# Kernel tuning notes

Hardware: AMD Instinct MI355X
Metric: run time of the kernel (lower is better)

The kernel has to match this reference:

```python
import jax, jax.numpy as jnp
import numpy as np

# model dims
N = 512        # node_size (ROIs)
S = 64         # sampling_size
TRS = 20       # TRs_per_window
STEPS = 20     # steps_per_TR = tr / step_size
DT = 0.05      # step_size (s)

# fixed Wong-Wang / Balloon-Windkessel constants (var=0 params in ParamsModel)
W_E, W_I = 1.0, 0.7
TAU_E, TAU_I = 0.1, 0.01
GAMMA_E, GAMMA_I = 0.641, 1.0
I_0, I_EXT = 0.32, 0.02
A_E, B_E, D_E = 310.0, 125.0, 0.16
A_I, B_I, D_I = 615.0, 177.0, 0.087
ALPHA, RHO = 0.32, 0.34
K1, K2, K3 = 2.38, 2.0, 0.48
V0, E0 = 0.02, 0.34
TAU_S, TAU_F, TAU_0 = 0.65, 0.41, 0.98


def h_tf(a, b, d, z):
    # abs-regularized sigmoid transfer (a*z-b)/(1-exp(-d*(a*z-b)))
    x = a * z - b
    return (1e-5 + jnp.abs(x)) / (1e-5 * d + jnp.abs(1.0 - jnp.exp(-d * x)))


def setup_inputs() -> dict:
    key = jax.random.key(0)
    ks = jax.random.split(key, 8)
    sc = jax.random.uniform(ks[0], (N, N), dtype=jnp.float32) * (1.0 - jnp.eye(N, dtype=jnp.float32))
    gains_con = 0.05 * jax.random.normal(ks[1], (N, N), dtype=jnp.float32)
    # hx: [N, 6] initial states (E, I, x, f, v, q)
    hx = jnp.concatenate([
        0.1 * jnp.ones((N, 2), jnp.float32),   # E, I
        jnp.zeros((N, 1), jnp.float32),        # x
        jnp.ones((N, 3), jnp.float32),         # f, v, q
    ], axis=1)
    hE = 0.1 * jnp.ones((N, 20), jnp.float32)
    external = jnp.zeros((N, STEPS, TRS), jnp.float32)
    noise_E0 = jax.random.normal(ks[2], (TRS, STEPS, N, S), dtype=jnp.float32)
    noise_I0 = jax.random.normal(ks[3], (TRS, STEPS, N, S), dtype=jnp.float32)
    noise_E = jax.random.normal(ks[4], (TRS, STEPS, N, S), dtype=jnp.float32)
    noise_I = jax.random.normal(ks[5], (TRS, STEPS, N, S), dtype=jnp.float32)
    noise_bold = jax.random.normal(ks[6], (TRS, N), dtype=jnp.float32)
    return dict(external=external, hx=hx, hE=hE, sc=sc, gains_con=gains_con,
                g=jnp.float32(20.0), g_EE=jnp.float32(3.5), g_IE=jnp.float32(0.42),
                g_EI=jnp.float32(0.42), std_in=jnp.float32(0.0), std_out=jnp.float32(0.02),
                noise_E0=noise_E0, noise_I0=noise_I0, noise_E=noise_E, noise_I=noise_I,
                noise_bold=noise_bold)


def reference(external, hx, hE, sc, gains_con, g, g_EE, g_IE, g_EI, std_in, std_out,
              noise_E0, noise_I0, noise_E, noise_I, noise_bold):
    relu = jax.nn.relu
    g_EE_e = 0.001 + relu(g_EE)
    g_IE_e = 0.001 + relu(g_IE)
    g_EI_e = 0.001 + relu(g_EI)
    std_in_e = 0.02 + relu(std_in)
    std_out_e = relu(std_out)
    # fitted, symmetrized, normalized SC -> Laplacian coupling
    sc_mod = jnp.exp(gains_con) * sc
    w = 0.5 * (sc_mod + sc_mod.T)
    w_n = w / jnp.linalg.norm(w)
    lap = -jnp.diag(w_n.sum(1)) + w_n                      # [N, N]
    ext = jnp.transpose(external, (2, 1, 0))               # [TRS, STEPS, N]
    sqdt = jnp.sqrt(jnp.float32(DT))

    def micro(carry, xs):
        hxE, hxI, x, f, v, q = carry
        e0, i0, eE, eI, ex = xs
        E = hxE[:, None] + 0.02 * e0                       # [N, S]
        I = hxI[:, None] + 0.001 * i0
        IE = jnp.tanh(relu(W_E * I_0 + I_EXT * ex[:, None] + g_EE_e * E + g * (lap @ E) - g_IE_e * I))
        II = jnp.tanh(relu(W_I * I_0 + g_EI_e * E - I))
        rE = h_tf(A_E, B_E, D_E, IE)
        rI = h_tf(A_I, B_I, D_I, II)
        En = E + DT * (-E / TAU_E + GAMMA_E * (1.0 - E) * rE) + sqdt * std_in_e * eE
        In = I + DT * (-I / TAU_I + GAMMA_I * rI) + sqdt * std_in_e * eI
        E = jnp.tanh(relu(En))                             # dynamic boundary
        I = jnp.tanh(relu(In))
        Em = jnp.maximum(E.mean(1), 1e-5)                  # [N]
        Im = jnp.maximum(I.mean(1), 1e-5)
        # hemodynamic (balloon-windkessel) states
        v_a = v ** (1.0 / ALPHA)
        xn = x + DT * (Em - x / TAU_S - (f - 1.0) / TAU_F)
        fn = f + DT * x
        vn = v + DT * (f - v_a) / TAU_0
        qn = q + DT * (f * (1.0 - (1.0 - RHO) ** (1.0 / f)) / RHO - q * v_a / v) / TAU_0
        return (Em, Im, jnp.tanh(xn), 1.0 + jnp.tanh(fn - 1.0),
                1.0 + jnp.tanh(vn - 1.0), 1.0 + jnp.tanh(qn - 1.0)), None

    def tr_step(carry, xs):
        e0, i0, eE, eI, exs, eb = xs
        carry, _ = jax.lax.scan(micro, carry, (e0, i0, eE, eI, exs))
        Em, Im, x, f, v, q = carry
        bold = std_out_e * eb + 100.0 * V0 / E0 * (K1 * (1.0 - q) + K2 * (1.0 - q / v) + K3 * (1.0 - v))
        return carry, bold

    carry0 = (hx[:, 0], hx[:, 1], hx[:, 2], hx[:, 3], hx[:, 4], hx[:, 5])
    _, bolds = jax.lax.scan(tr_step, carry0, (noise_E0, noise_I0, noise_E, noise_I, ext, noise_bold))
    return bolds.T                                         # [N, TRS] simulated BOLD window
```

## Files before the change

kernel.cpp:

```cpp
#include <hip/hip_runtime.h>
#include <hip/hip_bf16.h>

#define NN 512
#define SSAMP 64
#define NSTEP 400

__device__ __forceinline__ float wsum(float v){
  v += __shfl_xor(v, 32, 64);
  v += __shfl_xor(v, 16, 64);
  v += __shfl_xor(v,  8, 64);
  v += __shfl_xor(v,  4, 64);
  v += __shfl_xor(v,  2, 64);
  v += __shfl_xor(v,  1, 64);
  return v;
}
__device__ __forceinline__ float tanh_pos(float u){
  float e = __expf(2.0f*u);
  return 1.0f - 2.0f/(e+1.0f);
}
__device__ __forceinline__ float tanh_gen(float u){
  float a = fabsf(u);
  float e = __expf(2.0f*a);
  float t = 1.0f - 2.0f/(e+1.0f);
  return copysignf(t, u);
}
__device__ __forceinline__ float h_tf(float a, float b, float d, float z){
  float x = fmaf(a, z, -b);
  float num = 1e-5f + fabsf(x);
  float den = 1e-5f*d + fabsf(1.0f - __expf(-d*x));
  return num/den;
}

__device__ __forceinline__ float l0_load(const float* p){ return *p; }
__device__ __forceinline__ float l0_load(const __hip_bfloat16* p){ return __bfloat162float(*p); }
__device__ __forceinline__ void  l0_store(float* p, float v){ *p = v; }
__device__ __forceinline__ void  l0_store(__hip_bfloat16* p, float v){ *p = __float2bfloat16(v); }

#define F4ELEM(v,m) ((m)==0?(v).x:(m)==1?(v).y:(m)==2?(v).z:(v).w)

__global__ __launch_bounds__(256) void prep_w_kernel(
    const float* __restrict__ sc, const float* __restrict__ gc,
    float* __restrict__ w, float* __restrict__ normsq){
  int idx = blockIdx.x*256 + threadIdx.x;
  int i = idx >> 9, j = idx & 511;
  float a = __expf(gc[idx])*sc[idx];
  float b = __expf(gc[j*NN+i])*sc[j*NN+i];
  float wij = 0.5f*(a + b);
  w[idx] = wij;
  float p = wsum(wij*wij);
  if ((threadIdx.x & 63) == 0) atomicAdd(normsq, p);
}

__global__ __launch_bounds__(64) void prep_lap_kernel(
    const float* __restrict__ w, const float* __restrict__ normsq,
    float* __restrict__ lap){
  int i = blockIdx.x;
  int l = threadIdx.x;
  float vals[8]; float s = 0.f;
  #pragma unroll
  for (int j=0;j<8;j++){ vals[j] = w[i*NN + j*64 + l]; s += vals[j]; }
  float rs = wsum(s);
  float rn = 1.0f/sqrtf(normsq[0]);
  #pragma unroll
  for (int j=0;j<8;j++){
    int col = j*64 + l;
    float x = vals[j] - (col==i ? rs : 0.0f);
    lap[i*NN+col] = x*rn;
  }
}

template<typename TL>
__global__ __launch_bounds__(256) void gemm_kernel(
    const float* __restrict__ lap, const float* __restrict__ nE0,
    TL* __restrict__ L0){
  __shared__ __align__(16) float e0s[64][64];
  int t = blockIdx.y;
  int tid = threadIdx.x;
  int ts = tid & 7, tr = tid >> 3;
  int r0 = blockIdx.x*128 + tr*4;
  int s0 = ts*8;
  const float* e0t = nE0 + (size_t)t*NN*SSAMP;
  float acc[4][8];
  #pragma unroll
  for (int i=0;i<4;i++)
    #pragma unroll
    for (int j=0;j<8;j++) acc[i][j]=0.f;

  for (int kt=0; kt<8; ++kt){
    int kr = tid>>4, c4 = (tid&15)*4;
    const float* src = e0t + (size_t)(kt*64+kr)*SSAMP + c4;
    float4 a0 = *(const float4*)(src);
    float4 a1 = *(const float4*)(src + 16*SSAMP);
    float4 a2 = *(const float4*)(src + 32*SSAMP);
    float4 a3 = *(const float4*)(src + 48*SSAMP);
    __syncthreads();
    *(float4*)(&e0s[kr   ][c4]) = a0;
    *(float4*)(&e0s[kr+16][c4]) = a1;
    *(float4*)(&e0s[kr+32][c4]) = a2;
    *(float4*)(&e0s[kr+48][c4]) = a3;
    __syncthreads();
    const float* lb = lap + (size_t)r0*NN + kt*64;
    for (int kk=0; kk<64; kk+=4){
      float4 lq0 = *(const float4*)(lb +        kk);
      float4 lq1 = *(const float4*)(lb +   NN + kk);
      float4 lq2 = *(const float4*)(lb + 2*NN + kk);
      float4 lq3 = *(const float4*)(lb + 3*NN + kk);
      #pragma unroll
      for (int m=0;m<4;m++){
        float lm[4] = {F4ELEM(lq0,m), F4ELEM(lq1,m), F4ELEM(lq2,m), F4ELEM(lq3,m)};
        float4 ea = *(const float4*)(&e0s[kk+m][s0]);
        float4 eb = *(const float4*)(&e0s[kk+m][s0+4]);
        float ev[8] = {ea.x,ea.y,ea.z,ea.w, eb.x,eb.y,eb.z,eb.w};
        #pragma unroll
        for (int i=0;i<4;i++)
          #pragma unroll
          for (int j=0;j<8;j++)
            acc[i][j] = fmaf(lm[i], ev[j], acc[i][j]);
      }
    }
  }
  #pragma unroll
  for (int i=0;i<4;i++){
    TL* dst = L0 + ((size_t)t*NN + r0 + i)*SSAMP + s0;
    #pragma unroll
    for (int j=0;j<8;j++) l0_store(&dst[j], acc[i][j]);
  }
}

template<typename TL>
__global__ __launch_bounds__(256) void seq_kernel(
    const float* __restrict__ external, const float* __restrict__ hx,
    const float* __restrict__ lap, const TL* __restrict__ L0,
    const float* __restrict__ nE0, const float* __restrict__ nI0,
    const float* __restrict__ nE,  const float* __restrict__ nI,
    const float* __restrict__ nB,
    const float* __restrict__ gp,   const float* __restrict__ gEEp,
    const float* __restrict__ gIEp, const float* __restrict__ gEIp,
    const float* __restrict__ stdinp, const float* __restrict__ stdoutp,
    unsigned long long* __restrict__ xbuf,
    float* __restrict__ out)
{
  __shared__ float hxs[NN];
  const int tid  = threadIdx.x;
  const int wv   = tid >> 6, lane = tid & 63;
  const int n    = blockIdx.x*4 + wv;

  const float g    = gp[0];
  const float gEE  = 0.001f + fmaxf(gEEp[0], 0.f);
  const float gIE  = 0.001f + fmaxf(gIEp[0], 0.f);
  const float gEI  = 0.001f + fmaxf(gEIp[0], 0.f);
  const float sdin = 0.02f  + fmaxf(stdinp[0], 0.f);
  const float sdout=          fmaxf(stdoutp[0], 0.f);
  const float sqin = 0.22360679774997896f * sdin;

  float hxE = hx[n*6+0], hxI = hx[n*6+1];
  float xs  = hx[n*6+2], fs  = hx[n*6+3], vs = hx[n*6+4], qs = hx[n*6+5];

  if (lane==0){
    unsigned long long pk = (1ULL<<32) | (unsigned long long)__float_as_uint(hxE);
    __hip_atomic_store(&xbuf[n], pk, __ATOMIC_RELAXED, __HIP_MEMORY_SCOPE_AGENT);
  }

  const size_t nsbase = (size_t)n*SSAMP + lane;
  float c_e0 = nE0[nsbase];
  float c_i0 = nI0[nsbase];
  float c_eE = nE [nsbase];
  float c_eI = nI [nsbase];
  float c_L0 = l0_load(&L0[nsbase]);
  float c_ex = external[n*400 + 0];

  const float* laprow = lap + (size_t)n*NN;

  #pragma unroll 1
  for (int t=0; t<NSTEP; ++t){
    int tn = (t+1 < NSTEP) ? t+1 : t;
    size_t offn = (size_t)tn*NN*SSAMP + nsbase;
    float p_e0 = nE0[offn], p_i0 = nI0[offn], p_eE = nE[offn], p_eI = nI[offn];
    float p_L0 = l0_load(&L0[offn]);
    float p_ex = external[n*400 + (tn%20)*20 + (tn/20)];

    float E = fmaf(0.02f , c_e0, hxE);
    float I = fmaf(0.001f, c_i0, hxI);
    float II = tanh_pos(fmaxf(fmaf(gEI, E, 0.224f) - I, 0.f));
    float rI = h_tf(615.0f, 177.0f, 0.087f, II);
    float In = I + 0.05f*fmaf(-100.0f, I, rI) + sqin*c_eI;
    float Ip = tanh_pos(fmaxf(In, 0.f));
    float Im = fmaxf(wsum(Ip)*0.015625f, 1e-5f);
    float IEpre = 0.32f + 0.02f*c_ex + gEE*E + g*0.02f*c_L0 - gIE*I;

    const unsigned long long want = (unsigned long long)(t+1);
    unsigned long long* bc = xbuf + (size_t)(t&1)*NN;
    unsigned long long u0, u1;
    for(;;){
      u0 = __hip_atomic_load(&bc[tid],     __ATOMIC_RELAXED, __HIP_MEMORY_SCOPE_AGENT);
      u1 = __hip_atomic_load(&bc[tid+256], __ATOMIC_RELAXED, __HIP_MEMORY_SCOPE_AGENT);
      int ok = (int)(((u0>>32)==want) & ((u1>>32)==want));
      if (__syncthreads_and(ok)) break;
    }
    hxs[tid]     = __uint_as_float((unsigned int)u0);
    hxs[tid+256] = __uint_as_float((unsigned int)u1);
    __syncthreads();

    float mv = 0.f;
    #pragma unroll
    for (int j=0;j<8;j++) mv = fmaf(laprow[j*64+lane], hxs[j*64+lane], mv);
    float lapHx = wsum(mv);

    float IE = tanh_pos(fmaxf(fmaf(g, lapHx, IEpre), 0.f));
    float rE = h_tf(310.0f, 125.0f, 0.16f, IE);
    float En = E + 0.05f*fmaf(0.641f*(1.0f-E), rE, -10.0f*E) + sqin*c_eE;
    float Ep = tanh_pos(fmaxf(En, 0.f));
    float Em = fmaxf(wsum(Ep)*0.015625f, 1e-5f);

    if (lane==0){
      unsigned long long pk = ((unsigned long long)(t+2)<<32)
                            | (unsigned long long)__float_as_uint(Em);
      __hip_atomic_store(&xbuf[(size_t)((t+1)&1)*NN + n], pk,
                         __ATOMIC_RELAXED, __HIP_MEMORY_SCOPE_AGENT);
    }

    float va = __expf(3.125f*__logf(vs));
    float xn = xs + 0.05f*(Em - xs*1.5384615384615385f - (fs-1.0f)*2.4390243902439024f);
    float fn = fs + 0.05f*xs;
    float vn = vs + 0.05f*(fs - va)*1.0204081632653061f;
    float qn = qs + 0.05f*( fs*(1.0f - __expf(-0.41551544396166582f/fs))*2.9411764705882355f
                            - qs*va/vs )*1.0204081632653061f;
    xs = tanh_gen(xn);
    fs = 1.0f + tanh_gen(fn - 1.0f);
    vs = 1.0f + tanh_gen(vn - 1.0f);
    qs = 1.0f + tanh_gen(qn - 1.0f);
    hxE = Em; hxI = Im;

    if (((t+1) % 20) == 0 && lane==0){
      int tr = t/20;
      float eb = nB[tr*NN + n];
      float bold = sdout*eb + 5.882352941176471f*( 2.38f*(1.0f-qs)
                   + 2.0f*(1.0f - qs/vs) + 0.48f*(1.0f-vs) );
      out[n*20 + tr] = bold;
    }

    c_e0=p_e0; c_i0=p_i0; c_eE=p_eE; c_eI=p_eI; c_L0=p_L0; c_ex=p_ex;
  }
}

extern "C" void kernel_launch(void* const* d_in, const int* in_sizes, int n_in,
                              void* d_out, int out_size, void* d_ws, size_t ws_size,
                              hipStream_t stream) {
  (void)in_sizes; (void)n_in; (void)out_size;
  const float* external = (const float*)d_in[0];
  const float* hx   = (const float*)d_in[1];
  const float* sc   = (const float*)d_in[3];
  const float* gc   = (const float*)d_in[4];
  const float* gp   = (const float*)d_in[5];
  const float* gEE  = (const float*)d_in[6];
  const float* gIE  = (const float*)d_in[7];
  const float* gEI  = (const float*)d_in[8];
  const float* stdi = (const float*)d_in[9];
  const float* stdo = (const float*)d_in[10];
  const float* nE0  = (const float*)d_in[11];
  const float* nI0  = (const float*)d_in[12];
  const float* nE   = (const float*)d_in[13];
  const float* nI   = (const float*)d_in[14];
  const float* nB   = (const float*)d_in[15];
  float* out = (float*)d_out;

  char* ws = (char*)d_ws;
  float* normsq = (float*)ws;
  unsigned long long* xbuf = (unsigned long long*)(ws + 256);
  float* w   = (float*)(ws + 16384);
  float* lap = (float*)(ws + 16384 + (1<<20));
  char*  l0p = ws + 16384 + (2<<20);

  hipMemsetAsync(ws, 0, 16384, stream);
  prep_w_kernel  <<<1024, 256, 0, stream>>>(sc, gc, w, normsq);
  prep_lap_kernel<<< 512,  64, 0, stream>>>(w, normsq, lap);

  size_t l0_f32  = (size_t)NSTEP*NN*SSAMP*sizeof(float);
  size_t need_f32 = 16384 + (2<<20) + l0_f32;
  if (ws_size >= need_f32){
    gemm_kernel<float><<<dim3(4,NSTEP), 256, 0, stream>>>(lap, nE0, (float*)l0p);
    seq_kernel<float><<<128, 256, 0, stream>>>(external, hx, lap, (const float*)l0p,
        nE0, nI0, nE, nI, nB, gp, gEE, gIE, gEI, stdi, stdo, xbuf, out);
  } else {
    gemm_kernel<__hip_bfloat16><<<dim3(4,NSTEP), 256, 0, stream>>>(lap, nE0, (__hip_bfloat16*)l0p);
    seq_kernel<__hip_bfloat16><<<128, 256, 0, stream>>>(external, hx, lap, (const __hip_bfloat16*)l0p,
        nE0, nI0, nE, nI, nB, gp, gEE, gIE, gEI, stdi, stdo, xbuf, out);
  }
}
```

Before: 1.157 ms.

## Use bf16 MFMA precompute GEMM and a dedicated poller wave in sequential kernel

```diff
diff --git a/kernel.cpp b/kernel.cpp
--- a/kernel.cpp
+++ b/kernel.cpp
@@ -4,6 +4,11 @@
 #define NN 512
 #define SSAMP 64
 #define NSTEP 400
+#define CW 8
+#define SEQBLK 64
+
+typedef __attribute__((ext_vector_type(4))) float f32x4;
+typedef __attribute__((ext_vector_type(8))) short s16x8;
 
 __device__ __forceinline__ float wsum(float v){
   v += __shfl_xor(v, 32, 64);
@@ -30,13 +35,6 @@
   float den = 1e-5f*d + fabsf(1.0f - __expf(-d*x));
   return num/den;
 }
-
-__device__ __forceinline__ float l0_load(const float* p){ return *p; }
-__device__ __forceinline__ float l0_load(const __hip_bfloat16* p){ return __bfloat162float(*p); }
-__device__ __forceinline__ void  l0_store(float* p, float v){ *p = v; }
-__device__ __forceinline__ void  l0_store(__hip_bfloat16* p, float v){ *p = __float2bfloat16(v); }
-
-#define F4ELEM(v,m) ((m)==0?(v).x:(m)==1?(v).y:(m)==2?(v).z:(v).w)
 
 __global__ __launch_bounds__(256) void prep_w_kernel(
     const float* __restrict__ sc, const float* __restrict__ gc,
@@ -69,68 +67,76 @@
   }
 }
 
-template<typename TL>
-__global__ __launch_bounds__(256) void gemm_kernel(
-    const float* __restrict__ lap, const float* __restrict__ nE0,
-    TL* __restrict__ L0){
-  __shared__ __align__(16) float e0s[64][64];
+__global__ __launch_bounds__(256) void lap_bf_kernel(
+    const float* __restrict__ lap, __hip_bfloat16* __restrict__ lb){
+  int i = blockIdx.x*256 + threadIdx.x;
+  lb[i] = __float2bfloat16(lap[i]);
+}
+
+__global__ __launch_bounds__(256) void e0t_kernel(
+    const float* __restrict__ nE0, __hip_bfloat16* __restrict__ th){
+  __shared__ float tile[64][65];
+  int t = blockIdx.y, c = blockIdx.x;
+  const float* src = nE0 + ((size_t)t*NN + c*64)*SSAMP;
+  int tid = threadIdx.x;
+  int r0 = tid>>2, c4 = (tid&3)*16;
+  #pragma unroll
+  for (int i=0;i<4;i++){
+    float4 v = *(const float4*)(src + r0*64 + c4 + i*4);
+    tile[r0][c4+i*4+0]=v.x; tile[r0][c4+i*4+1]=v.y;
+    tile[r0][c4+i*4+2]=v.z; tile[r0][c4+i*4+3]=v.w;
+  }
+  __syncthreads();
+  int s = tid>>2, nseg = (tid&3)*16;
+  __hip_bfloat16 hs[16];
+  #pragma unroll
+  for (int i=0;i<16;i++) hs[i] = __float2bfloat16(tile[nseg+i][s]);
+  size_t doff = ((size_t)t*64 + s)*NN + c*64 + nseg;
+  *(uint4*)(th + doff)     = *(uint4*)&hs[0];
+  *(uint4*)(th + doff + 8) = *(uint4*)&hs[8];
+}
+
+__global__ __launch_bounds__(256) void mfma_gemm_kernel(
+    const __hip_bfloat16* __restrict__ A, const __hip_bfloat16* __restrict__ B,
+    __hip_bfloat16* __restrict__ L0){
   int t = blockIdx.y;
-  int tid = threadIdx.x;
-  int ts = tid & 7, tr = tid >> 3;
-  int r0 = blockIdx.x*128 + tr*4;
-  int s0 = ts*8;
-  const float* e0t = nE0 + (size_t)t*NN*SSAMP;
-  float acc[4][8];
-  #pragma unroll
-  for (int i=0;i<4;i++)
-    #pragma unroll
-    for (int j=0;j<8;j++) acc[i][j]=0.f;
-
-  for (int kt=0; kt<8; ++kt){
-    int kr = tid>>4, c4 = (tid&15)*4;
-    const float* src = e0t + (size_t)(kt*64+kr)*SSAMP + c4;
-    float4 a0 = *(const float4*)(src);
-    float4 a1 = *(const float4*)(src + 16*SSAMP);
-    float4 a2 = *(const float4*)(src + 32*SSAMP);
-    float4 a3 = *(const float4*)(src + 48*SSAMP);
-    __syncthreads();
-    *(float4*)(&e0s[kr   ][c4]) = a0;
-    *(float4*)(&e0s[kr+16][c4]) = a1;
-    *(float4*)(&e0s[kr+32][c4]) = a2;
-    *(float4*)(&e0s[kr+48][c4]) = a3;
-    __syncthreads();
-    const float* lb = lap + (size_t)r0*NN + kt*64;
-    for (int kk=0; kk<64; kk+=4){
-      float4 lq0 = *(const float4*)(lb +        kk);
-      float4 lq1 = *(const float4*)(lb +   NN + kk);
-      float4 lq2 = *(const float4*)(lb + 2*NN + kk);
-      float4 lq3 = *(const float4*)(lb + 3*NN + kk);
+  int nb = blockIdx.x;
+  int w  = threadIdx.x>>6, l = threadIdx.x&63;
+  int lr = l&15, lg = l>>4;
+  f32x4 acc[4][2] = {};
+  const short* ap = (const short*)A + ((size_t)t*64 + lr)*NN + lg*8;
+  int col0 = nb*128 + w*32 + lr;
+  const short* bp = (const short*)B + (size_t)col0*NN + lg*8;
+  for (int k0=0; k0<NN; k0+=32){
+    s16x8 a[4], b[2];
+    #pragma unroll
+    for (int mt=0;mt<4;mt++) a[mt] = *(const s16x8*)(ap + mt*16*NN + k0);
+    #pragma unroll
+    for (int nt=0;nt<2;nt++) b[nt] = *(const s16x8*)(bp + nt*16*NN + k0);
+    #pragma unroll
+    for (int mt=0;mt<4;mt++)
       #pragma unroll
-      for (int m=0;m<4;m++){
-        float lm[4] = {F4ELEM(lq0,m), F4ELEM(lq1,m), F4ELEM(lq2,m), F4ELEM(lq3,m)};
-        float4 ea = *(const float4*)(&e0s[kk+m][s0]);
-        float4 eb = *(const float4*)(&e0s[kk+m][s0+4]);
-        float ev[8] = {ea.x,ea.y,ea.z,ea.w, eb.x,eb.y,eb.z,eb.w};
-        #pragma unroll
-        for (int i=0;i<4;i++)
-          #pragma unroll
-          for (int j=0;j<8;j++)
-            acc[i][j] = fmaf(lm[i], ev[j], acc[i][j]);
-      }
+      for (int nt=0;nt<2;nt++)
+        acc[mt][nt] = __builtin_amdgcn_mfma_f32_16x16x32_bf16(a[mt], b[nt], acc[mt][nt],0,0,0);
+  }
+  #pragma unroll
+  for (int mt=0;mt<4;mt++)
+    #pragma unroll
+    for (int nt=0;nt<2;nt++){
+      int n = col0 + nt*16;
+      int s = mt*16 + lg*4;
+      ushort4 h;
+      h.x = __hip_bfloat16_raw(__float2bfloat16(acc[mt][nt].x)).x;
+      h.y = __hip_bfloat16_raw(__float2bfloat16(acc[mt][nt].y)).x;
+      h.z = __hip_bfloat16_raw(__float2bfloat16(acc[mt][nt].z)).x;
+      h.w = __hip_bfloat16_raw(__float2bfloat16(acc[mt][nt].w)).x;
+      *(ushort4*)((unsigned short*)L0 + ((size_t)t*NN + n)*SSAMP + s) = h;
     }
-  }
-  #pragma unroll
-  for (int i=0;i<4;i++){
-    TL* dst = L0 + ((size_t)t*NN + r0 + i)*SSAMP + s0;
-    #pragma unroll
-    for (int j=0;j<8;j++) l0_store(&dst[j], acc[i][j]);
-  }
-}
-
-template<typename TL>
-__global__ __launch_bounds__(256) void seq_kernel(
+}
+
+__global__ __launch_bounds__(576) void seq_kernel(
     const float* __restrict__ external, const float* __restrict__ hx,
-    const float* __restrict__ lap, const TL* __restrict__ L0,
+    const float* __restrict__ lap, const __hip_bfloat16* __restrict__ L0,
     const float* __restrict__ nE0, const float* __restrict__ nI0,
     const float* __restrict__ nE,  const float* __restrict__ nI,
     const float* __restrict__ nB,
@@ -140,10 +146,39 @@
     unsigned long long* __restrict__ xbuf,
     float* __restrict__ out)
 {
-  __shared__ float hxs[NN];
+  __shared__ float hxs[2][NN];
+  __shared__ int flag;
   const int tid  = threadIdx.x;
   const int wv   = tid >> 6, lane = tid & 63;
-  const int n    = blockIdx.x*4 + wv;
+  if (tid == 0) flag = 0;
+
+  if (wv == CW){
+    __syncthreads();
+    #pragma unroll 1
+    for (int t=0; t<NSTEP; ++t){
+      const unsigned want = (unsigned)(t+1);
+      unsigned long long* bc = xbuf + (size_t)(t&1)*NN;
+      unsigned long long u[8];
+      for(;;){
+        #pragma unroll
+        for (int j=0;j<8;j++)
+          u[j] = __hip_atomic_load(&bc[j*64+lane], __ATOMIC_RELAXED, __HIP_MEMORY_SCOPE_AGENT);
+        int ok = 1;
+        #pragma unroll
+        for (int j=0;j<8;j++) ok &= (int)((unsigned)(u[j]>>32) == want);
+        if (__all(ok)) break;
+        __builtin_amdgcn_s_sleep(1);
+      }
+      #pragma unroll
+      for (int j=0;j<8;j++)
+        hxs[t&1][j*64+lane] = __uint_as_float((unsigned)u[j]);
+      if (lane==0)
+        __hip_atomic_store(&flag, t+1, __ATOMIC_RELEASE, __HIP_MEMORY_SCOPE_WORKGROUP);
+    }
+    return;
+  }
+
+  const int n = blockIdx.x*CW + wv;
 
   const float g    = gp[0];
   const float gEE  = 0.001f + fmaxf(gEEp[0], 0.f);
@@ -156,27 +191,30 @@
   float hxE = hx[n*6+0], hxI = hx[n*6+1];
   float xs  = hx[n*6+2], fs  = hx[n*6+3], vs = hx[n*6+4], qs = hx[n*6+5];
 
-  if (lane==0){
-    unsigned long long pk = (1ULL<<32) | (unsigned long long)__float_as_uint(hxE);
-    __hip_atomic_store(&xbuf[n], pk, __ATOMIC_RELAXED, __HIP_MEMORY_SCOPE_AGENT);
-  }
+  float lr[8];
+  #pragma unroll
+  for (int j=0;j<8;j++) lr[j] = lap[(size_t)n*NN + j*64 + lane];
+
+  if (lane==0)
+    __hip_atomic_store(&xbuf[n], (1ULL<<32) | (unsigned long long)__float_as_uint(hxE),
+                       __ATOMIC_RELAXED, __HIP_MEMORY_SCOPE_AGENT);
 
   const size_t nsbase = (size_t)n*SSAMP + lane;
   float c_e0 = nE0[nsbase];
   float c_i0 = nI0[nsbase];
   float c_eE = nE [nsbase];
   float c_eI = nI [nsbase];
-  float c_L0 = l0_load(&L0[nsbase]);
+  float c_L0 = __bfloat162float(L0[nsbase]);
   float c_ex = external[n*400 + 0];
 
-  const float* laprow = lap + (size_t)n*NN;
+  __syncthreads();
 
   #pragma unroll 1
   for (int t=0; t<NSTEP; ++t){
     int tn = (t+1 < NSTEP) ? t+1 : t;
     size_t offn = (size_t)tn*NN*SSAMP + nsbase;
     float p_e0 = nE0[offn], p_i0 = nI0[offn], p_eE = nE[offn], p_eI = nI[offn];
-    float p_L0 = l0_load(&L0[offn]);
+    float p_L0 = __bfloat162float(L0[offn]);
     float p_ex = external[n*400 + (tn%20)*20 + (tn/20)];
 
     float E = fmaf(0.02f , c_e0, hxE);
@@ -188,22 +226,11 @@
     float Im = fmaxf(wsum(Ip)*0.015625f, 1e-5f);
     float IEpre = 0.32f + 0.02f*c_ex + gEE*E + g*0.02f*c_L0 - gIE*I;
 
-    const unsigned long long want = (unsigned long long)(t+1);
-    unsigned long long* bc = xbuf + (size_t)(t&1)*NN;
-    unsigned long long u0, u1;
-    for(;;){
-      u0 = __hip_atomic_load(&bc[tid],     __ATOMIC_RELAXED, __HIP_MEMORY_SCOPE_AGENT);
-      u1 = __hip_atomic_load(&bc[tid+256], __ATOMIC_RELAXED, __HIP_MEMORY_SCOPE_AGENT);
-      int ok = (int)(((u0>>32)==want) & ((u1>>32)==want));
-      if (__syncthreads_and(ok)) break;
-    }
-    hxs[tid]     = __uint_as_float((unsigned int)u0);
-    hxs[tid+256] = __uint_as_float((unsigned int)u1);
-    __syncthreads();
+    while (__hip_atomic_load(&flag, __ATOMIC_ACQUIRE, __HIP_MEMORY_SCOPE_WORKGROUP) < t+1){}
 
     float mv = 0.f;
     #pragma unroll
-    for (int j=0;j<8;j++) mv = fmaf(laprow[j*64+lane], hxs[j*64+lane], mv);
+    for (int j=0;j<8;j++) mv = fmaf(lr[j], hxs[t&1][j*64+lane], mv);
     float lapHx = wsum(mv);
 
     float IE = tanh_pos(fmaxf(fmaf(g, lapHx, IEpre), 0.f));
@@ -212,12 +239,10 @@
     float Ep = tanh_pos(fmaxf(En, 0.f));
     float Em = fmaxf(wsum(Ep)*0.015625f, 1e-5f);
 
-    if (lane==0){
-      unsigned long long pk = ((unsigned long long)(t+2)<<32)
-                            | (unsigned long long)__float_as_uint(Em);
-      __hip_atomic_store(&xbuf[(size_t)((t+1)&1)*NN + n], pk,
+    if (lane==0)
+      __hip_atomic_store(&xbuf[(size_t)((t+1)&1)*NN + n],
+                         ((unsigned long long)(t+2)<<32) | (unsigned long long)__float_as_uint(Em),
                          __ATOMIC_RELAXED, __HIP_MEMORY_SCOPE_AGENT);
-    }
 
     float va = __expf(3.125f*__logf(vs));
     float xn = xs + 0.05f*(Em - xs*1.5384615384615385f - (fs-1.0f)*2.4390243902439024f);
@@ -246,7 +271,7 @@
 extern "C" void kernel_launch(void* const* d_in, const int* in_sizes, int n_in,
                               void* d_out, int out_size, void* d_ws, size_t ws_size,
                               hipStream_t stream) {
-  (void)in_sizes; (void)n_in; (void)out_size;
+  (void)in_sizes; (void)n_in; (void)out_size; (void)ws_size;
   const float* external = (const float*)d_in[0];
   const float* hx   = (const float*)d_in[1];
   const float* sc   = (const float*)d_in[3];
@@ -265,25 +290,22 @@
   float* out = (float*)d_out;
 
   char* ws = (char*)d_ws;
-  float* normsq = (float*)ws;
+  const size_t MB = 1048576;
+  float*    normsq = (float*)ws;
   unsigned long long* xbuf = (unsigned long long*)(ws + 256);
-  float* w   = (float*)(ws + 16384);
-  float* lap = (float*)(ws + 16384 + (1<<20));
-  char*  l0p = ws + 16384 + (2<<20);
+  float* lap            = (float*)(ws + 16384);
+  __hip_bfloat16* lapbf = (__hip_bfloat16*)(ws + 16384 + 1*MB);
+  char* thp             = ws + 16384 + 1*MB + 512*1024;
+  float* w              = (float*)thp;
+  __hip_bfloat16* th    = (__hip_bfloat16*)thp;
+  __hip_bfloat16* L0    = (__hip_bfloat16*)(thp + (size_t)NSTEP*64*NN*2);
 
   hipMemsetAsync(ws, 0, 16384, stream);
   prep_w_kernel  <<<1024, 256, 0, stream>>>(sc, gc, w, normsq);
   prep_lap_kernel<<< 512,  64, 0, stream>>>(w, normsq, lap);
-
-  size_t l0_f32  = (size_t)NSTEP*NN*SSAMP*sizeof(float);
-  size_t need_f32 = 16384 + (2<<20) + l0_f32;
-  if (ws_size >= need_f32){
-    gemm_kernel<float><<<dim3(4,NSTEP), 256, 0, stream>>>(lap, nE0, (float*)l0p);
-    seq_kernel<float><<<128, 256, 0, stream>>>(external, hx, lap, (const float*)l0p,
-        nE0, nI0, nE, nI, nB, gp, gEE, gIE, gEI, stdi, stdo, xbuf, out);
-  } else {
-    gemm_kernel<__hip_bfloat16><<<dim3(4,NSTEP), 256, 0, stream>>>(lap, nE0, (__hip_bfloat16*)l0p);
-    seq_kernel<__hip_bfloat16><<<128, 256, 0, stream>>>(external, hx, lap, (const __hip_bfloat16*)l0p,
-        nE0, nI0, nE, nI, nB, gp, gEE, gIE, gEI, stdi, stdo, xbuf, out);
-  }
-}
+  lap_bf_kernel  <<<1024, 256, 0, stream>>>(lap, lapbf);
+  e0t_kernel     <<<dim3(8, NSTEP), 256, 0, stream>>>(nE0, th);
+  mfma_gemm_kernel<<<dim3(4, NSTEP), 256, 0, stream>>>(th, lapbf, L0);
+  seq_kernel<<<SEQBLK, 576, 0, stream>>>(external, hx, lap, L0,
+      nE0, nI0, nE, nI, nB, gp, gEE, gIE, gEI, stdi, stdo, xbuf, out);
+}
```

New measurement: 1.604 ms. 38.6% more time.
